# Kernel optimization log

Measured on AMD Instinct MI355X. Metric: run time of the kernel, lower is better.

Reference implementation:

```python
import jax, jax.numpy as jnp
import numpy as np

DIMS = 1024; HEAD = 16; HD = DIMS // HEAD
MAX_DIST = 1024; MAX_SPAN = 1024; TEMP_SCALE = 0.01
SCALE = HD ** -0.25  # hd^-0.25 per the torch modules


def _layer_norm(x, g, b, eps=1e-5):
    m = jnp.mean(x, -1, keepdims=True)
    v = jnp.mean((x - m) ** 2, -1, keepdims=True)
    return (x - m) * jax.lax.rsqrt(v + eps) * g + b


def _forward(x, ln_a_g, ln_a_b, ln_b_g, ln_b_b, Wq, bq, Wk, Wv, bv, Wc, bc, Wp, bp, Wo, bo):
    B, S, D = x.shape
    local = _layer_norm(x, ln_a_g, ln_a_b)
    globe = _layer_norm(x, ln_b_g, ln_b_b)
    # --- global path: QueryModule/KeyModule/ValueModule + AttentionCombiner SDPA (mask=None) ---
    q = (globe @ Wq.T + bq).reshape(B, S, HEAD, HD).transpose(0, 2, 1, 3) * SCALE
    k = (globe @ Wk.T).reshape(B, S, HEAD, HD).transpose(0, 2, 1, 3) * SCALE
    v = (globe @ Wv.T + bv).reshape(B, S, HEAD, HD).transpose(0, 2, 1, 3)
    # SDPA applies its own 1/sqrt(hd) on top of the modules' hd^-0.25 scalings (faithful to torch)
    scores = jnp.einsum('bhqd,bhkd->bhqk', q, k) / jnp.sqrt(jnp.asarray(HD, x.dtype))
    w = jax.nn.softmax(scores, -1)
    g_out = jnp.einsum('bhqk,bhkd->bhqd', w, v).transpose(0, 2, 1, 3).reshape(B, S, D)
    g_out = g_out @ Wc.T + bc
    # --- span predictor; torch uses span_scale.mean().item() which detaches -> stop_gradient ---
    span_scale = jax.nn.sigmoid(jnp.mean(g_out, 1) @ Wp.T + bp)  # [B,1]
    span_mean = jax.lax.stop_gradient(jnp.mean(span_scale))
    span_len = jnp.minimum(jnp.floor(MAX_SPAN * span_mean).astype(jnp.int32), S)
    eff = jnp.maximum(jnp.minimum(span_len, MAX_DIST), 1)  # eff_span (>=1 to keep softmax finite)
    temp = 1.0 + TEMP_SCALE * (1.0 - span_mean)  # sharpen=True branch
    # --- local AdaptiveSpan path: q[:, :eff], k[:, :eff], v[:, :eff] expressed as masking
    #     so shapes stay static under jit; rows >= eff are the zero-padding of the span output.
    lh = local.reshape(B, S, HEAD, HD).transpose(0, 2, 1, 3)  # [B,H,S,hd]
    ls = jnp.einsum('bhqd,bhkd->bhqk', lh, lh) / temp * SCALE
    valid = jnp.arange(S) < eff
    ls = jnp.where(valid[None, None, None, :], ls, jnp.asarray(-1e30, x.dtype))
    lw = jax.nn.softmax(ls, -1)
    l_out = jnp.einsum('bhqk,bhkd->bhqd', lw, lh).transpose(0, 2, 1, 3).reshape(B, S, D)
    l_out = jnp.where(valid[None, :, None], l_out, jnp.asarray(0.0, x.dtype))
    combined = jnp.concatenate([l_out, g_out], -1)  # [B,S,2D]
    return combined @ Wo.T + bo


def setup_inputs() -> dict:
    key = jax.random.key(0)
    ks = jax.random.split(key, 8)
    B, S = 2, 1024
    nrm = lambda k, sh, std=0.02: jax.random.normal(k, sh, jnp.float32) * std
    return {
        'x': jax.random.normal(ks[0], (B, S, DIMS), jnp.float32),
        'ln_a_g': jnp.ones(DIMS, jnp.float32), 'ln_a_b': jnp.zeros(DIMS, jnp.float32),
        'ln_b_g': jnp.ones(DIMS, jnp.float32), 'ln_b_b': jnp.zeros(DIMS, jnp.float32),
        'Wq': nrm(ks[1], (DIMS, DIMS)), 'bq': jnp.zeros(DIMS, jnp.float32),
        'Wk': nrm(ks[2], (DIMS, DIMS)),
        'Wv': nrm(ks[3], (DIMS, DIMS)), 'bv': jnp.zeros(DIMS, jnp.float32),
        'Wc': nrm(ks[4], (DIMS, DIMS)), 'bc': jnp.zeros(DIMS, jnp.float32),
        'Wp': nrm(ks[5], (1, DIMS), (2.0 / (DIMS + 1)) ** 0.5), 'bp': jnp.zeros(1, jnp.float32),
        'Wo': nrm(ks[6], (DIMS, 2 * DIMS)), 'bo': jnp.zeros(DIMS, jnp.float32),
    }


def reference(x, ln_a_g, ln_a_b, ln_b_g, ln_b_b, Wq, bq, Wk, Wv, bv, Wc, bc, Wp, bp, Wo, bo):
    return _forward(x, ln_a_g, ln_a_b, ln_b_g, ln_b_b, Wq, bq, Wk, Wv, bv, Wc, bc, Wp, bp, Wo, bo)
```

## Files before the change

kernel.cpp:

```cpp
#include <hip/hip_runtime.h>
#include <math.h>

#define S_LEN 1024
#define DIMS  1024
#define NHEAD 16
#define HD    64
#define BATCH 2
#define MROWS (BATCH * S_LEN)

typedef unsigned short us;
typedef __attribute__((ext_vector_type(8))) __bf16 bf8_t;
typedef __attribute__((ext_vector_type(8))) unsigned short us8_t;
typedef __attribute__((ext_vector_type(4))) unsigned short us4_t;
typedef __attribute__((ext_vector_type(4))) float f32x4;

static __device__ inline us f2bf(float f) {
    unsigned int u = __builtin_bit_cast(unsigned int, f);
    unsigned int r = u + 0x7fffu + ((u >> 16) & 1u);
    return (us)(r >> 16);
}
static __device__ inline float bf2f(us v) {
    unsigned int u = ((unsigned int)v) << 16;
    return __builtin_bit_cast(float, u);
}
static __device__ inline f32x4 mfma16(us8_t a, us8_t b, f32x4 c) {
    return __builtin_amdgcn_mfma_f32_16x16x32_bf16(
        __builtin_bit_cast(bf8_t, a), __builtin_bit_cast(bf8_t, b), c, 0, 0, 0);
}

__global__ __launch_bounds__(256) void cvt5_kernel(
    const float* __restrict__ s0, const float* __restrict__ s1,
    const float* __restrict__ s2, const float* __restrict__ s3,
    const float* __restrict__ s4,
    us* __restrict__ d0, us* __restrict__ d1, us* __restrict__ d2,
    us* __restrict__ d3, us* __restrict__ d4)
{
    int bidx = blockIdx.x;
    const float* src; us* dst; int blk;
    if (bidx < 1024)      { src = s0; dst = d0; blk = bidx; }
    else if (bidx < 2048) { src = s1; dst = d1; blk = bidx - 1024; }
    else if (bidx < 3072) { src = s2; dst = d2; blk = bidx - 2048; }
    else if (bidx < 4096) { src = s3; dst = d3; blk = bidx - 3072; }
    else                  { src = s4; dst = d4; blk = bidx - 4096; }
    size_t idx = (size_t)blk * 1024 + threadIdx.x * 4;
    float4 v = *(const float4*)(src + idx);
    us4_t ot;
    ot[0] = f2bf(v.x); ot[1] = f2bf(v.y); ot[2] = f2bf(v.z); ot[3] = f2bf(v.w);
    *(us4_t*)(dst + idx) = ot;
}

__global__ __launch_bounds__(256) void ln2_kernel(
    const float* __restrict__ x,
    const float* __restrict__ ga, const float* __restrict__ ba,
    const float* __restrict__ gb, const float* __restrict__ bb,
    us* __restrict__ outA, us* __restrict__ outB)
{
    int row = blockIdx.x;
    int t = threadIdx.x;
    const float* xr = x + (size_t)row * DIMS;
    float4 v = *(const float4*)(xr + t * 4);
    float s  = v.x + v.y + v.z + v.w;
    float s2 = v.x * v.x + v.y * v.y + v.z * v.z + v.w * v.w;
#pragma unroll
    for (int o = 32; o > 0; o >>= 1) {
        s  += __shfl_down(s, o, 64);
        s2 += __shfl_down(s2, o, 64);
    }
    __shared__ float rs[4], rs2[4];
    int wid = t >> 6, lane = t & 63;
    if (lane == 0) { rs[wid] = s; rs2[wid] = s2; }
    __syncthreads();
    float S0 = rs[0] + rs[1] + rs[2] + rs[3];
    float S2 = rs2[0] + rs2[1] + rs2[2] + rs2[3];
    float mean = S0 * (1.0f / DIMS);
    float var  = S2 * (1.0f / DIMS) - mean * mean;
    float inv  = 1.0f / sqrtf(var + 1e-5f);
    float4 vga = *(const float4*)(ga + t * 4);
    float4 vba = *(const float4*)(ba + t * 4);
    float4 vgb = *(const float4*)(gb + t * 4);
    float4 vbb = *(const float4*)(bb + t * 4);
    float nx = (v.x - mean) * inv, ny = (v.y - mean) * inv;
    float nz = (v.z - mean) * inv, nw = (v.w - mean) * inv;
    us4_t oa, ob;
    oa[0] = f2bf(nx * vga.x + vba.x); oa[1] = f2bf(ny * vga.y + vba.y);
    oa[2] = f2bf(nz * vga.z + vba.z); oa[3] = f2bf(nw * vga.w + vba.w);
    ob[0] = f2bf(nx * vgb.x + vbb.x); ob[1] = f2bf(ny * vgb.y + vbb.y);
    ob[2] = f2bf(nz * vgb.z + vbb.z); ob[3] = f2bf(nw * vgb.w + vbb.w);
    *(us4_t*)(outA + (size_t)row * DIMS + t * 4) = oa;
    *(us4_t*)(outB + (size_t)row * DIMS + t * 4) = ob;
}

template <int OUTBF>
static __device__ __forceinline__ void gemm_body(
    const us* __restrict__ A, int lda,
    const us* __restrict__ W, int ldw,
    const float* __restrict__ bias,
    void* __restrict__ Cp, int ldc, int K,
    int bm, int bn, us* As, us* Bs)
{
    int tid = threadIdx.x;
    int w = tid >> 6, l = tid & 63, l15 = l & 15, lhi = l >> 4;
    int wr = w >> 1, wc = w & 1;
    f32x4 acc[2][2] = {{{0,0,0,0},{0,0,0,0}},{{0,0,0,0},{0,0,0,0}}};
    int srow = tid >> 3;
    int scol8 = tid & 7;
    const us* Ap = A + (size_t)(bm + srow) * lda + scol8 * 8;
    const us* Wpt = W + (size_t)(bn + srow) * ldw + scol8 * 8;
    int sl = (scol8 ^ (srow & 7)) * 8;
    us8_t a0 = *(const us8_t*)(Ap);
    us8_t a1 = *(const us8_t*)(Ap + (size_t)32 * lda);
    us8_t b0 = *(const us8_t*)(Wpt);
    us8_t b1 = *(const us8_t*)(Wpt + (size_t)32 * ldw);
    for (int kt = 0; kt < K; kt += 64) {
        __syncthreads();
        *(us8_t*)&As[srow * 64 + sl] = a0;
        *(us8_t*)&As[(srow + 32) * 64 + sl] = a1;
        *(us8_t*)&Bs[srow * 64 + sl] = b0;
        *(us8_t*)&Bs[(srow + 32) * 64 + sl] = b1;
        __syncthreads();
        if (kt + 64 < K) {
            a0 = *(const us8_t*)(Ap + kt + 64);
            a1 = *(const us8_t*)(Ap + (size_t)32 * lda + kt + 64);
            b0 = *(const us8_t*)(Wpt + kt + 64);
            b1 = *(const us8_t*)(Wpt + (size_t)32 * ldw + kt + 64);
        }
#pragma unroll
        for (int kk = 0; kk < 2; ++kk) {
            us8_t af[2], bfr[2];
#pragma unroll
            for (int m = 0; m < 2; ++m) {
                int rowm = wr * 32 + m * 16 + l15;
                af[m] = *(const us8_t*)&As[rowm * 64 + (((kk * 4 + lhi)) ^ (rowm & 7)) * 8];
            }
#pragma unroll
            for (int n = 0; n < 2; ++n) {
                int rown = wc * 32 + n * 16 + l15;
                bfr[n] = *(const us8_t*)&Bs[rown * 64 + (((kk * 4 + lhi)) ^ (rown & 7)) * 8];
            }
#pragma unroll
            for (int m = 0; m < 2; ++m)
#pragma unroll
                for (int n = 0; n < 2; ++n)
                    acc[m][n] = mfma16(af[m], bfr[n], acc[m][n]);
        }
    }
    float bvv[2] = {0.f, 0.f};
    if (bias) {
#pragma unroll
        for (int n = 0; n < 2; ++n)
            bvv[n] = bias[bn + wc * 32 + n * 16 + l15];
    }
#pragma unroll
    for (int m = 0; m < 2; ++m) {
#pragma unroll
        for (int n = 0; n < 2; ++n) {
#pragma unroll
            for (int r = 0; r < 4; ++r) {
                int row = bm + wr * 32 + m * 16 + lhi * 4 + r;
                int col = bn + wc * 32 + n * 16 + l15;
                float val = acc[m][n][r] + bvv[n];
                if (OUTBF) ((us*)Cp)[(size_t)row * ldc + col] = f2bf(val);
                else       ((float*)Cp)[(size_t)row * ldc + col] = val;
            }
        }
    }
}

template <int OUTBF>
__global__ __launch_bounds__(256) void gemm_bf16(
    const us* __restrict__ A, int lda,
    const us* __restrict__ W, int ldw,
    const float* __restrict__ bias,
    void* __restrict__ Cp, int ldc, int K)
{
    __shared__ __align__(16) us As[64 * 64];
    __shared__ __align__(16) us Bs[64 * 64];
    gemm_body<OUTBF>(A, lda, W, ldw, bias, Cp, ldc, K,
                     blockIdx.y * 64, blockIdx.x * 64, As, Bs);
}

__global__ __launch_bounds__(256) void gemm_qkv(
    const us* __restrict__ A,
    const us* __restrict__ Wq, const us* __restrict__ Wk, const us* __restrict__ Wv,
    const float* __restrict__ bq, const float* __restrict__ bv,
    us* __restrict__ qo, us* __restrict__ ko, us* __restrict__ vo)
{
    __shared__ __align__(16) us As[64 * 64];
    __shared__ __align__(16) us Bs[64 * 64];
    int which = blockIdx.x >> 4;
    int bn = (blockIdx.x & 15) * 64, bm = blockIdx.y * 64;
    const us* W = (which == 0) ? Wq : ((which == 1) ? Wk : Wv);
    const float* bias = (which == 0) ? bq : ((which == 2) ? bv : nullptr);
    us* Out = (which == 0) ? qo : ((which == 1) ? ko : vo);
    gemm_body<1>(A, DIMS, W, DIMS, bias, Out, DIMS, DIMS, bm, bn, As, Bs);
}

template <int LOCAL>
__global__ __launch_bounds__(512) void attn_mfma(
    const us* __restrict__ Q, const us* __restrict__ K,
    const us* __restrict__ V, us* __restrict__ O, int ldo,
    const float* __restrict__ span)
{
    __shared__ __align__(16) us Ks[2][64 * 64];
    __shared__ __align__(16) us Vt[2][64 * 64];
    __shared__ __align__(16) us Ps[8][16 * 64];

    int b = blockIdx.z, h = blockIdx.y;
    int q0blk = blockIdx.x * 64;
    int tid = threadIdx.x;
    int w = tid >> 6, l = tid & 63;
    int l15 = l & 15, lhi = l >> 4;
    int wq = w & 3, wk = w >> 2;

    float scale; int eff;
    if (LOCAL) { scale = span[1]; eff = (int)span[0]; }
    else       { scale = 1.0f / 64.0f; eff = S_LEN; }
    int ntiles = LOCAL ? ((eff + 63) >> 6) : 16;
    int nIter = (ntiles + 1) >> 1;

    int qrow = q0blk + wq * 16 + l15;
    const us* qptr = Q + ((size_t)(b * S_LEN + qrow)) * DIMS + h * HD + lhi * 8;
    us8_t qf[2];
    qf[0] = *(const us8_t*)(qptr);
    qf[1] = *(const us8_t*)(qptr + 32);

    f32x4 o[4] = {{0,0,0,0},{0,0,0,0},{0,0,0,0},{0,0,0,0}};
    float m_r[4] = {-1e30f, -1e30f, -1e30f, -1e30f};
    float l_r[4] = {0.f, 0.f, 0.f, 0.f};

    int half = tid >> 8;
    int t0 = tid & 255;
    int krow = t0 >> 3, kcol8 = t0 & 7;
    int ksl = (kcol8 ^ (krow & 7)) * 8;
    int vkb = t0 & 15, vdb = t0 >> 4;
    const us* Kb = K + ((size_t)(b * S_LEN)) * DIMS + h * HD;
    const us* Vb = V + ((size_t)(b * S_LEN)) * DIMS + h * HD;

    us8_t kc0, kc1;
    us4_t vr0, vr1, vr2, vr3;
    if (half < ntiles) {
        const us* kp = Kb + (size_t)(half * 64 + krow) * DIMS + kcol8 * 8;
        kc0 = *(const us8_t*)kp;
        kc1 = *(const us8_t*)(kp + (size_t)32 * DIMS);
        const us* vp = Vb + (size_t)(half * 64 + vkb * 4) * DIMS + vdb * 4;
        vr0 = *(const us4_t*)(vp);
        vr1 = *(const us4_t*)(vp + DIMS);
        vr2 = *(const us4_t*)(vp + 2 * DIMS);
        vr3 = *(const us4_t*)(vp + 3 * DIMS);
    }

    for (int i = 0; i < nIter; ++i) {
        __syncthreads();
        if (2 * i + half < ntiles) {
            *(us8_t*)&Ks[half][krow * 64 + ksl] = kc0;
            *(us8_t*)&Ks[half][(krow + 32) * 64 + ksl] = kc1;
#pragma unroll
            for (int j = 0; j < 4; ++j) {
                int d = vdb * 4 + j;
                us4_t wv;
                wv[0] = vr0[j]; wv[1] = vr1[j]; wv[2] = vr2[j]; wv[3] = vr3[j];
                int slot = (vkb >> 1) ^ (d & 7);
                *(us4_t*)&Vt[half][d * 64 + slot * 8 + (vkb & 1) * 4] = wv;
            }
        }
        __syncthreads();
        int nt2 = 2 * (i + 1) + half;
        if (nt2 < ntiles) {
            const us* kp = Kb + (size_t)(nt2 * 64 + krow) * DIMS + kcol8 * 8;
            kc0 = *(const us8_t*)kp;
            kc1 = *(const us8_t*)(kp + (size_t)32 * DIMS);
            const us* vp = Vb + (size_t)(nt2 * 64 + vkb * 4) * DIMS + vdb * 4;
            vr0 = *(const us4_t*)(vp);
            vr1 = *(const us4_t*)(vp + DIMS);
            vr2 = *(const us4_t*)(vp + 2 * DIMS);
            vr3 = *(const us4_t*)(vp + 3 * DIMS);
        }
        int kt = 2 * i + wk;
        if (kt < ntiles) {
            f32x4 s4[4] = {{0,0,0,0},{0,0,0,0},{0,0,0,0},{0,0,0,0}};
            __builtin_amdgcn_s_setprio(1);
#pragma unroll
            for (int kk = 0; kk < 2; ++kk) {
#pragma unroll
                for (int n = 0; n < 4; ++n) {
                    int key = n * 16 + l15;
                    int slot = (kk * 4 + lhi) ^ (key & 7);
                    us8_t bk = *(const us8_t*)&Ks[wk][key * 64 + slot * 8];
                    s4[n] = mfma16(qf[kk], bk, s4[n]);
                }
            }
            __builtin_amdgcn_s_setprio(0);
#pragma unroll
            for (int n = 0; n < 4; ++n) {
                s4[n] *= scale;
                if (LOCAL) {
                    int key = kt * 64 + n * 16 + l15;
                    if (key >= eff) {
                        s4[n][0] = -1e30f; s4[n][1] = -1e30f;
                        s4[n][2] = -1e30f; s4[n][3] = -1e30f;
                    }
                }
            }
            float tm[4];
#pragma unroll
            for (int r = 0; r < 4; ++r)
                tm[r] = fmaxf(fmaxf(s4[0][r], s4[1][r]), fmaxf(s4[2][r], s4[3][r]));
#pragma unroll
            for (int msk = 1; msk <= 8; msk <<= 1) {
#pragma unroll
                for (int r = 0; r < 4; ++r)
                    tm[r] = fmaxf(tm[r], __shfl_xor(tm[r], msk, 64));
            }
            bool upd = (tm[0] > m_r[0] + 8.f) || (tm[1] > m_r[1] + 8.f) ||
                       (tm[2] > m_r[2] + 8.f) || (tm[3] > m_r[3] + 8.f);
            if (upd) {
                float fac[4];
#pragma unroll
                for (int r = 0; r < 4; ++r) {
                    float mn = fmaxf(m_r[r], tm[r]);
                    fac[r] = __expf(m_r[r] - mn);
                    m_r[r] = mn;
                    l_r[r] *= fac[r];
                }
#pragma unroll
                for (int n = 0; n < 4; ++n) {
                    o[n][0] *= fac[0]; o[n][1] *= fac[1];
                    o[n][2] *= fac[2]; o[n][3] *= fac[3];
                }
            }
            float ladd[4] = {0.f, 0.f, 0.f, 0.f};
#pragma unroll
            for (int n = 0; n < 4; ++n) {
                int col = n * 16 + l15;
                int slotbase = col >> 3;
#pragma unroll
                for (int r = 0; r < 4; ++r) {
                    float p = __expf(s4[n][r] - m_r[r]);
                    ladd[r] += p;
                    int qlr = lhi * 4 + r;
                    int slot = slotbase ^ (qlr & 7);
                    Ps[w][qlr * 64 + slot * 8 + (col & 7)] = f2bf(p);
                }
            }
#pragma unroll
            for (int msk = 1; msk <= 8; msk <<= 1) {
#pragma unroll
                for (int r = 0; r < 4; ++r)
                    ladd[r] += __shfl_xor(ladd[r], msk, 64);
            }
#pragma unroll
            for (int r = 0; r < 4; ++r) l_r[r] += ladd[r];

            __builtin_amdgcn_s_setprio(1);
#pragma unroll
            for (int kk = 0; kk < 2; ++kk) {
                int slot = (kk * 4 + lhi) ^ (l15 & 7);
                us8_t pa = *(const us8_t*)&Ps[w][l15 * 64 + slot * 8];
#pragma unroll
                for (int n = 0; n < 4; ++n) {
                    int d = n * 16 + l15;
                    int vslot = (kk * 4 + lhi) ^ (d & 7);
                    us8_t vb = *(const us8_t*)&Vt[wk][d * 64 + vslot * 8];
                    o[n] = mfma16(pa, vb, o[n]);
                }
            }
            __builtin_amdgcn_s_setprio(0);
        }
    }

    __syncthreads();
    float* obuf = (float*)&Ks[0][0];
    float* mlb  = (float*)&Vt[0][0];
    if (wk == 1) {
#pragma unroll
        for (int n = 0; n < 4; ++n)
#pragma unroll
            for (int r = 0; r < 4; ++r)
                obuf[wq * 1024 + (lhi * 4 + r) * 64 + n * 16 + l15] = o[n][r];
        if (l15 == 0) {
#pragma unroll
            for (int r = 0; r < 4; ++r) {
                mlb[wq * 32 + (lhi * 4 + r) * 2 + 0] = m_r[r];
                mlb[wq * 32 + (lhi * 4 + r) * 2 + 1] = l_r[r];
            }
        }
    }
    __syncthreads();
    if (wk == 0) {
        float f0[4], f1[4], rcp[4];
#pragma unroll
        for (int r = 0; r < 4; ++r) {
            int row = lhi * 4 + r;
            float m1 = mlb[wq * 32 + row * 2 + 0];
            float l1 = mlb[wq * 32 + row * 2 + 1];
            float ms = fmaxf(m_r[r], m1);
            f0[r] = __expf(m_r[r] - ms);
            f1[r] = __expf(m1 - ms);
            rcp[r] = 1.0f / (l_r[r] * f0[r] + l1 * f1[r]);
        }
#pragma unroll
        for (int n = 0; n < 4; ++n) {
#pragma unroll
            for (int r = 0; r < 4; ++r) {
                int row = q0blk + wq * 16 + lhi * 4 + r;
                float val = (o[n][r] * f0[r] +
                             obuf[wq * 1024 + (lhi * 4 + r) * 64 + n * 16 + l15] * f1[r]) * rcp[r];
                if (LOCAL && row >= eff) val = 0.0f;
                O[((size_t)(b * S_LEN + row)) * ldo + h * HD + n * 16 + l15] = f2bf(val);
            }
        }
    }
}

__global__ __launch_bounds__(256) void span1_kernel(
    const us* __restrict__ gout, const float* __restrict__ Wp,
    float* __restrict__ partials)
{
    int slice = blockIdx.x;
    int b = blockIdx.y;
    int t = threadIdx.x;
    float4 wp = *(const float4*)(Wp + t * 4);
    float acc = 0;
    int s0 = slice * 128;
    for (int s = s0; s < s0 + 128; ++s) {
        us4_t g = *(const us4_t*)(gout + (size_t)(b * S_LEN + s) * 2048 + t * 4);
        acc += bf2f(g[0]) * wp.x + bf2f(g[1]) * wp.y + bf2f(g[2]) * wp.z + bf2f(g[3]) * wp.w;
    }
#pragma unroll
    for (int o = 32; o > 0; o >>= 1) acc += __shfl_down(acc, o, 64);
    __shared__ float r[4];
    int wid = t >> 6, lane = t & 63;
    if (lane == 0) r[wid] = acc;
    __syncthreads();
    if (t == 0) partials[b * 8 + slice] = r[0] + r[1] + r[2] + r[3];
}

__global__ void span2_kernel(const float* __restrict__ partials,
                             const float* __restrict__ bp,
                             float* __restrict__ spanbuf)
{
    if (threadIdx.x == 0 && blockIdx.x == 0) {
        float l0 = 0, l1 = 0;
        for (int i = 0; i < 8; ++i) { l0 += partials[i]; l1 += partials[8 + i]; }
        l0 = l0 * (1.0f / 1024.0f) + bp[0];
        l1 = l1 * (1.0f / 1024.0f) + bp[0];
        float s0 = 1.0f / (1.0f + expf(-l0));
        float s1 = 1.0f / (1.0f + expf(-l1));
        float sm = 0.5f * (s0 + s1);
        int sl = (int)floorf(1024.0f * sm);
        int eff = sl; if (eff > 1024) eff = 1024; if (eff < 1) eff = 1;
        float temp = 1.0f + 0.01f * (1.0f - sm);
        spanbuf[0] = (float)eff;
        spanbuf[1] = 0.35355339059327378f / temp;
    }
}

extern "C" void kernel_launch(void* const* d_in, const int* in_sizes, int n_in,
                              void* d_out, int out_size, void* d_ws, size_t ws_size,
                              hipStream_t stream)
{
    (void)in_sizes; (void)n_in; (void)out_size; (void)ws_size;
    const float* x   = (const float*)d_in[0];
    const float* lag = (const float*)d_in[1];
    const float* lab = (const float*)d_in[2];
    const float* lbg = (const float*)d_in[3];
    const float* lbb = (const float*)d_in[4];
    const float* Wq  = (const float*)d_in[5];
    const float* bq  = (const float*)d_in[6];
    const float* Wk  = (const float*)d_in[7];
    const float* Wv  = (const float*)d_in[8];
    const float* bv  = (const float*)d_in[9];
    const float* Wc  = (const float*)d_in[10];
    const float* bc  = (const float*)d_in[11];
    const float* Wp  = (const float*)d_in[12];
    const float* bp  = (const float*)d_in[13];
    const float* Wo  = (const float*)d_in[14];
    const float* bo  = (const float*)d_in[15];
    float* out = (float*)d_out;
    us* wsu = (us*)d_ws;

    const size_t NM = (size_t)MROWS * DIMS;
    us* lnAbf = wsu;
    us* lnBbf = wsu + NM;
    us* gattbf = lnBbf;
    us* qbf   = wsu + 2 * NM;
    us* kbf   = wsu + 3 * NM;
    us* vbf   = wsu + 4 * NM;
    us* combbf = qbf;
    us* Wqbf  = wsu + 5 * NM;
    us* Wkbf  = Wqbf + DIMS * DIMS;
    us* Wvbf  = Wkbf + DIMS * DIMS;
    us* Wcbf  = Wvbf + DIMS * DIMS;
    us* Wobf  = Wcbf + DIMS * DIMS;
    float* partials = (float*)(Wobf + 2 * DIMS * DIMS);
    float* spanbuf  = partials + 16;

    cvt5_kernel<<<6144, 256, 0, stream>>>(Wq, Wk, Wv, Wc, Wo,
                                          Wqbf, Wkbf, Wvbf, Wcbf, Wobf);

    ln2_kernel<<<MROWS, 256, 0, stream>>>(x, lag, lab, lbg, lbb, lnAbf, lnBbf);

    gemm_qkv<<<dim3(48, MROWS / 64), 256, 0, stream>>>(
        lnBbf, Wqbf, Wkbf, Wvbf, bq, bv, qbf, kbf, vbf);

    dim3 ag(S_LEN / 64, NHEAD, BATCH);
    attn_mfma<0><<<ag, 512, 0, stream>>>(qbf, kbf, vbf, gattbf, DIMS, nullptr);

    dim3 gg(DIMS / 64, MROWS / 64);
    gemm_bf16<1><<<gg, 256, 0, stream>>>(gattbf, DIMS, Wcbf, DIMS, bc, combbf + 1024, 2048, DIMS);

    span1_kernel<<<dim3(8, BATCH), 256, 0, stream>>>(combbf + 1024, Wp, partials);
    span2_kernel<<<1, 64, 0, stream>>>(partials, bp, spanbuf);

    attn_mfma<1><<<ag, 512, 0, stream>>>(lnAbf, lnAbf, lnAbf, combbf, 2048, spanbuf);

    gemm_bf16<0><<<gg, 256, 0, stream>>>(combbf, 2048, Wobf, 2048, bo, out, DIMS, 2 * DIMS);
}
```

Before: 142.2 us.

## Use 128-row GEMM tiles, exp2 softmax, packed bf16 converts, deferred row-sum reduction

Adds a 128x64 GEMM tile variant and uses it for the QKV and output projections, so each block reuses its weight tile across twice as many rows. In attention, the scale is folded with log2(e) so softmax can use exp2, and the lazy-rescale threshold is adjusted to match. The per-tile cross-lane row-sum shuffle is moved to a single reduction after the loop. Fp32-to-bf16 conversion now uses the packed v_cvt_pk_bf16_f32 instruction, and swizzle address arithmetic is simplified. The larger tiles halve the block count and raise register pressure, which may lower occupancy.

Result: no change. 143.7 us (+1.1%).

```diff
diff --git a/kernel.cpp b/kernel.cpp
--- a/kernel.cpp
+++ b/kernel.cpp
@@ -7,6 +7,7 @@
 #define HD    64
 #define BATCH 2
 #define MROWS (BATCH * S_LEN)
+#define LOG2E 1.44269504088896f
 
 typedef unsigned short us;
 typedef __attribute__((ext_vector_type(8))) __bf16 bf8_t;
@@ -22,6 +23,11 @@
 static __device__ inline float bf2f(us v) {
     unsigned int u = ((unsigned int)v) << 16;
     return __builtin_bit_cast(float, u);
+}
+static __device__ inline unsigned int pk2bf(float lo, float hi) {
+    unsigned int r;
+    asm("v_cvt_pk_bf16_f32 %0, %1, %2" : "=v"(r) : "v"(lo), "v"(hi));
+    return r;
 }
 static __device__ inline f32x4 mfma16(us8_t a, us8_t b, f32x4 c) {
     return __builtin_amdgcn_mfma_f32_16x16x32_bf16(
@@ -91,7 +97,7 @@
 }
 
 template <int OUTBF>
-static __device__ __forceinline__ void gemm_body(
+static __device__ __forceinline__ void gemm128_body(
     const us* __restrict__ A, int lda,
     const us* __restrict__ W, int ldw,
     const float* __restrict__ bias,
@@ -101,6 +107,127 @@
     int tid = threadIdx.x;
     int w = tid >> 6, l = tid & 63, l15 = l & 15, lhi = l >> 4;
     int wr = w >> 1, wc = w & 1;
+    f32x4 acc[4][2];
+#pragma unroll
+    for (int m = 0; m < 4; ++m) { acc[m][0] = (f32x4){0,0,0,0}; acc[m][1] = (f32x4){0,0,0,0}; }
+    int srow = tid >> 3;
+    int scol8 = tid & 7;
+    int sl = (scol8 ^ (srow & 7)) * 8;
+    const us* Ap = A + (size_t)(bm + srow) * lda + scol8 * 8;
+    const us* Wpt = W + (size_t)(bn + srow) * ldw + scol8 * 8;
+    us8_t a0 = *(const us8_t*)(Ap);
+    us8_t a1 = *(const us8_t*)(Ap + (size_t)32 * lda);
+    us8_t a2 = *(const us8_t*)(Ap + (size_t)64 * lda);
+    us8_t a3 = *(const us8_t*)(Ap + (size_t)96 * lda);
+    us8_t b0 = *(const us8_t*)(Wpt);
+    us8_t b1 = *(const us8_t*)(Wpt + (size_t)32 * ldw);
+    int xorbase = l15 & 7;
+    for (int kt = 0; kt < K; kt += 64) {
+        __syncthreads();
+        *(us8_t*)&As[(srow +  0) * 64 + sl] = a0;
+        *(us8_t*)&As[(srow + 32) * 64 + sl] = a1;
+        *(us8_t*)&As[(srow + 64) * 64 + sl] = a2;
+        *(us8_t*)&As[(srow + 96) * 64 + sl] = a3;
+        *(us8_t*)&Bs[(srow +  0) * 64 + sl] = b0;
+        *(us8_t*)&Bs[(srow + 32) * 64 + sl] = b1;
+        __syncthreads();
+        if (kt + 64 < K) {
+            a0 = *(const us8_t*)(Ap + kt + 64);
+            a1 = *(const us8_t*)(Ap + (size_t)32 * lda + kt + 64);
+            a2 = *(const us8_t*)(Ap + (size_t)64 * lda + kt + 64);
+            a3 = *(const us8_t*)(Ap + (size_t)96 * lda + kt + 64);
+            b0 = *(const us8_t*)(Wpt + kt + 64);
+            b1 = *(const us8_t*)(Wpt + (size_t)32 * ldw + kt + 64);
+        }
+#pragma unroll
+        for (int kk = 0; kk < 2; ++kk) {
+            int xo = ((kk * 4 + lhi) ^ xorbase) * 8;
+            us8_t af[4], bfr[2];
+#pragma unroll
+            for (int m = 0; m < 4; ++m)
+                af[m] = *(const us8_t*)&As[(wr * 64 + m * 16 + l15) * 64 + xo];
+#pragma unroll
+            for (int n = 0; n < 2; ++n)
+                bfr[n] = *(const us8_t*)&Bs[(wc * 32 + n * 16 + l15) * 64 + xo];
+#pragma unroll
+            for (int m = 0; m < 4; ++m)
+#pragma unroll
+                for (int n = 0; n < 2; ++n)
+                    acc[m][n] = mfma16(af[m], bfr[n], acc[m][n]);
+        }
+    }
+    float bvv[2] = {0.f, 0.f};
+    if (bias) {
+#pragma unroll
+        for (int n = 0; n < 2; ++n)
+            bvv[n] = bias[bn + wc * 32 + n * 16 + l15];
+    }
+#pragma unroll
+    for (int m = 0; m < 4; ++m) {
+#pragma unroll
+        for (int n = 0; n < 2; ++n) {
+            int row = bm + wr * 64 + m * 16 + lhi * 4;
+            int col = bn + wc * 32 + n * 16 + l15;
+            if (OUTBF) {
+                us* Cb = (us*)Cp;
+                unsigned int p01 = pk2bf(acc[m][n][0] + bvv[n], acc[m][n][1] + bvv[n]);
+                unsigned int p23 = pk2bf(acc[m][n][2] + bvv[n], acc[m][n][3] + bvv[n]);
+                Cb[(size_t)(row + 0) * ldc + col] = (us)p01;
+                Cb[(size_t)(row + 1) * ldc + col] = (us)(p01 >> 16);
+                Cb[(size_t)(row + 2) * ldc + col] = (us)p23;
+                Cb[(size_t)(row + 3) * ldc + col] = (us)(p23 >> 16);
+            } else {
+                float* Cf = (float*)Cp;
+#pragma unroll
+                for (int r = 0; r < 4; ++r)
+                    Cf[(size_t)(row + r) * ldc + col] = acc[m][n][r] + bvv[n];
+            }
+        }
+    }
+}
+
+template <int OUTBF>
+__global__ __launch_bounds__(256) void gemm128(
+    const us* __restrict__ A, int lda,
+    const us* __restrict__ W, int ldw,
+    const float* __restrict__ bias,
+    void* __restrict__ Cp, int ldc, int K)
+{
+    __shared__ __align__(16) us As[128 * 64];
+    __shared__ __align__(16) us Bs[64 * 64];
+    gemm128_body<OUTBF>(A, lda, W, ldw, bias, Cp, ldc, K,
+                        blockIdx.y * 128, blockIdx.x * 64, As, Bs);
+}
+
+__global__ __launch_bounds__(256) void gemm_qkv(
+    const us* __restrict__ A,
+    const us* __restrict__ Wq, const us* __restrict__ Wk, const us* __restrict__ Wv,
+    const float* __restrict__ bq, const float* __restrict__ bv,
+    us* __restrict__ qo, us* __restrict__ ko, us* __restrict__ vo)
+{
+    __shared__ __align__(16) us As[128 * 64];
+    __shared__ __align__(16) us Bs[64 * 64];
+    int which = blockIdx.x >> 4;
+    int bn = (blockIdx.x & 15) * 64, bm = blockIdx.y * 128;
+    const us* W = (which == 0) ? Wq : ((which == 1) ? Wk : Wv);
+    const float* bias = (which == 0) ? bq : ((which == 2) ? bv : nullptr);
+    us* Out = (which == 0) ? qo : ((which == 1) ? ko : vo);
+    gemm128_body<1>(A, DIMS, W, DIMS, bias, Out, DIMS, DIMS, bm, bn, As, Bs);
+}
+
+template <int OUTBF>
+__global__ __launch_bounds__(256) void gemm_bf16(
+    const us* __restrict__ A, int lda,
+    const us* __restrict__ W, int ldw,
+    const float* __restrict__ bias,
+    void* __restrict__ Cp, int ldc, int K)
+{
+    __shared__ __align__(16) us As[64 * 64];
+    __shared__ __align__(16) us Bs[64 * 64];
+    int tid = threadIdx.x;
+    int w = tid >> 6, l = tid & 63, l15 = l & 15, lhi = l >> 4;
+    int wr = w >> 1, wc = w & 1;
+    int bm = blockIdx.y * 64, bn = blockIdx.x * 64;
     f32x4 acc[2][2] = {{{0,0,0,0},{0,0,0,0}},{{0,0,0,0},{0,0,0,0}}};
     int srow = tid >> 3;
     int scol8 = tid & 7;
@@ -111,6 +238,7 @@
     us8_t a1 = *(const us8_t*)(Ap + (size_t)32 * lda);
     us8_t b0 = *(const us8_t*)(Wpt);
     us8_t b1 = *(const us8_t*)(Wpt + (size_t)32 * ldw);
+    int xorbase = l15 & 7;
     for (int kt = 0; kt < K; kt += 64) {
         __syncthreads();
         *(us8_t*)&As[srow * 64 + sl] = a0;
@@ -126,17 +254,14 @@
         }
 #pragma unroll
         for (int kk = 0; kk < 2; ++kk) {
+            int xo = ((kk * 4 + lhi) ^ xorbase) * 8;
             us8_t af[2], bfr[2];
 #pragma unroll
-            for (int m = 0; m < 2; ++m) {
-                int rowm = wr * 32 + m * 16 + l15;
-                af[m] = *(const us8_t*)&As[rowm * 64 + (((kk * 4 + lhi)) ^ (rowm & 7)) * 8];
-            }
-#pragma unroll
-            for (int n = 0; n < 2; ++n) {
-                int rown = wc * 32 + n * 16 + l15;
-                bfr[n] = *(const us8_t*)&Bs[rown * 64 + (((kk * 4 + lhi)) ^ (rown & 7)) * 8];
-            }
+            for (int m = 0; m < 2; ++m)
+                af[m] = *(const us8_t*)&As[(wr * 32 + m * 16 + l15) * 64 + xo];
+#pragma unroll
+            for (int n = 0; n < 2; ++n)
+                bfr[n] = *(const us8_t*)&Bs[(wc * 32 + n * 16 + l15) * 64 + xo];
 #pragma unroll
             for (int m = 0; m < 2; ++m)
 #pragma unroll
@@ -154,45 +279,24 @@
     for (int m = 0; m < 2; ++m) {
 #pragma unroll
         for (int n = 0; n < 2; ++n) {
-#pragma unroll
-            for (int r = 0; r < 4; ++r) {
-                int row = bm + wr * 32 + m * 16 + lhi * 4 + r;
-                int col = bn + wc * 32 + n * 16 + l15;
-                float val = acc[m][n][r] + bvv[n];
-                if (OUTBF) ((us*)Cp)[(size_t)row * ldc + col] = f2bf(val);
-                else       ((float*)Cp)[(size_t)row * ldc + col] = val;
-            }
-        }
-    }
-}
-
-template <int OUTBF>
-__global__ __launch_bounds__(256) void gemm_bf16(
-    const us* __restrict__ A, int lda,
-    const us* __restrict__ W, int ldw,
-    const float* __restrict__ bias,
-    void* __restrict__ Cp, int ldc, int K)
-{
-    __shared__ __align__(16) us As[64 * 64];
-    __shared__ __align__(16) us Bs[64 * 64];
-    gemm_body<OUTBF>(A, lda, W, ldw, bias, Cp, ldc, K,
-                     blockIdx.y * 64, blockIdx.x * 64, As, Bs);
-}
-
-__global__ __launch_bounds__(256) void gemm_qkv(
-    const us* __restrict__ A,
-    const us* __restrict__ Wq, const us* __restrict__ Wk, const us* __restrict__ Wv,
-    const float* __restrict__ bq, const float* __restrict__ bv,
-    us* __restrict__ qo, us* __restrict__ ko, us* __restrict__ vo)
-{
-    __shared__ __align__(16) us As[64 * 64];
-    __shared__ __align__(16) us Bs[64 * 64];
-    int which = blockIdx.x >> 4;
-    int bn = (blockIdx.x & 15) * 64, bm = blockIdx.y * 64;
-    const us* W = (which == 0) ? Wq : ((which == 1) ? Wk : Wv);
-    const float* bias = (which == 0) ? bq : ((which == 2) ? bv : nullptr);
-    us* Out = (which == 0) ? qo : ((which == 1) ? ko : vo);
-    gemm_body<1>(A, DIMS, W, DIMS, bias, Out, DIMS, DIMS, bm, bn, As, Bs);
+            int row = bm + wr * 32 + m * 16 + lhi * 4;
+            int col = bn + wc * 32 + n * 16 + l15;
+            if (OUTBF) {
+                us* Cb = (us*)Cp;
+                unsigned int p01 = pk2bf(acc[m][n][0] + bvv[n], acc[m][n][1] + bvv[n]);
+                unsigned int p23 = pk2bf(acc[m][n][2] + bvv[n], acc[m][n][3] + bvv[n]);
+                Cb[(size_t)(row + 0) * ldc + col] = (us)p01;
+                Cb[(size_t)(row + 1) * ldc + col] = (us)(p01 >> 16);
+                Cb[(size_t)(row + 2) * ldc + col] = (us)p23;
+                Cb[(size_t)(row + 3) * ldc + col] = (us)(p23 >> 16);
+            } else {
+                float* Cf = (float*)Cp;
+#pragma unroll
+                for (int r = 0; r < 4; ++r)
+                    Cf[(size_t)(row + r) * ldc + col] = acc[m][n][r] + bvv[n];
+            }
+        }
+    }
 }
 
 template <int LOCAL>
@@ -213,8 +317,8 @@
     int wq = w & 3, wk = w >> 2;
 
     float scale; int eff;
-    if (LOCAL) { scale = span[1]; eff = (int)span[0]; }
-    else       { scale = 1.0f / 64.0f; eff = S_LEN; }
+    if (LOCAL) { scale = span[1] * LOG2E; eff = (int)span[0]; }
+    else       { scale = LOG2E / 64.0f; eff = S_LEN; }
     int ntiles = LOCAL ? ((eff + 63) >> 6) : 16;
     int nIter = (ntiles + 1) >> 1;
 
@@ -281,11 +385,10 @@
             __builtin_amdgcn_s_setprio(1);
 #pragma unroll
             for (int kk = 0; kk < 2; ++kk) {
+                int xo = ((kk * 4 + lhi) ^ (l15 & 7)) * 8;
 #pragma unroll
                 for (int n = 0; n < 4; ++n) {
-                    int key = n * 16 + l15;
-                    int slot = (kk * 4 + lhi) ^ (key & 7);
-                    us8_t bk = *(const us8_t*)&Ks[wk][key * 64 + slot * 8];
+                    us8_t bk = *(const us8_t*)&Ks[wk][(n * 16 + l15) * 64 + xo];
                     s4[n] = mfma16(qf[kk], bk, s4[n]);
                 }
             }
@@ -311,14 +414,14 @@
                 for (int r = 0; r < 4; ++r)
                     tm[r] = fmaxf(tm[r], __shfl_xor(tm[r], msk, 64));
             }
-            bool upd = (tm[0] > m_r[0] + 8.f) || (tm[1] > m_r[1] + 8.f) ||
-                       (tm[2] > m_r[2] + 8.f) || (tm[3] > m_r[3] + 8.f);
+            bool upd = (tm[0] > m_r[0] + 11.5f) || (tm[1] > m_r[1] + 11.5f) ||
+                       (tm[2] > m_r[2] + 11.5f) || (tm[3] > m_r[3] + 11.5f);
             if (upd) {
                 float fac[4];
 #pragma unroll
                 for (int r = 0; r < 4; ++r) {
                     float mn = fmaxf(m_r[r], tm[r]);
-                    fac[r] = __expf(m_r[r] - mn);
+                    fac[r] = exp2f(m_r[r] - mn);
                     m_r[r] = mn;
                     l_r[r] *= fac[r];
                 }
@@ -328,44 +431,43 @@
                     o[n][2] *= fac[2]; o[n][3] *= fac[3];
                 }
             }
-            float ladd[4] = {0.f, 0.f, 0.f, 0.f};
 #pragma unroll
             for (int n = 0; n < 4; ++n) {
                 int col = n * 16 + l15;
                 int slotbase = col >> 3;
-#pragma unroll
-                for (int r = 0; r < 4; ++r) {
-                    float p = __expf(s4[n][r] - m_r[r]);
-                    ladd[r] += p;
-                    int qlr = lhi * 4 + r;
-                    int slot = slotbase ^ (qlr & 7);
-                    Ps[w][qlr * 64 + slot * 8 + (col & 7)] = f2bf(p);
-                }
-            }
-#pragma unroll
-            for (int msk = 1; msk <= 8; msk <<= 1) {
-#pragma unroll
-                for (int r = 0; r < 4; ++r)
-                    ladd[r] += __shfl_xor(ladd[r], msk, 64);
-            }
-#pragma unroll
-            for (int r = 0; r < 4; ++r) l_r[r] += ladd[r];
-
+                float p0 = exp2f(s4[n][0] - m_r[0]);
+                float p1 = exp2f(s4[n][1] - m_r[1]);
+                float p2 = exp2f(s4[n][2] - m_r[2]);
+                float p3 = exp2f(s4[n][3] - m_r[3]);
+                l_r[0] += p0; l_r[1] += p1; l_r[2] += p2; l_r[3] += p3;
+                unsigned int p01 = pk2bf(p0, p1);
+                unsigned int p23 = pk2bf(p2, p3);
+                int q0 = lhi * 4;
+                Ps[w][(q0 + 0) * 64 + ((slotbase ^ ((q0 + 0) & 7)) * 8) + (col & 7)] = (us)p01;
+                Ps[w][(q0 + 1) * 64 + ((slotbase ^ ((q0 + 1) & 7)) * 8) + (col & 7)] = (us)(p01 >> 16);
+                Ps[w][(q0 + 2) * 64 + ((slotbase ^ ((q0 + 2) & 7)) * 8) + (col & 7)] = (us)p23;
+                Ps[w][(q0 + 3) * 64 + ((slotbase ^ ((q0 + 3) & 7)) * 8) + (col & 7)] = (us)(p23 >> 16);
+            }
             __builtin_amdgcn_s_setprio(1);
 #pragma unroll
             for (int kk = 0; kk < 2; ++kk) {
-                int slot = (kk * 4 + lhi) ^ (l15 & 7);
-                us8_t pa = *(const us8_t*)&Ps[w][l15 * 64 + slot * 8];
+                int xo = ((kk * 4 + lhi) ^ (l15 & 7)) * 8;
+                us8_t pa = *(const us8_t*)&Ps[w][l15 * 64 + ((kk * 4 + lhi) ^ (l15 & 7)) * 8];
 #pragma unroll
                 for (int n = 0; n < 4; ++n) {
-                    int d = n * 16 + l15;
-                    int vslot = (kk * 4 + lhi) ^ (d & 7);
-                    us8_t vb = *(const us8_t*)&Vt[wk][d * 64 + vslot * 8];
+                    us8_t vb = *(const us8_t*)&Vt[wk][(n * 16 + l15) * 64 + xo];
                     o[n] = mfma16(pa, vb, o[n]);
                 }
             }
             __builtin_amdgcn_s_setprio(0);
         }
+    }
+
+#pragma unroll
+    for (int msk = 1; msk <= 8; msk <<= 1) {
+#pragma unroll
+        for (int r = 0; r < 4; ++r)
+            l_r[r] += __shfl_xor(l_r[r], msk, 64);
     }
 
     __syncthreads();
@@ -394,20 +496,29 @@
             float m1 = mlb[wq * 32 + row * 2 + 0];
             float l1 = mlb[wq * 32 + row * 2 + 1];
             float ms = fmaxf(m_r[r], m1);
-            f0[r] = __expf(m_r[r] - ms);
-            f1[r] = __expf(m1 - ms);
+            f0[r] = exp2f(m_r[r] - ms);
+            f1[r] = exp2f(m1 - ms);
             rcp[r] = 1.0f / (l_r[r] * f0[r] + l1 * f1[r]);
         }
 #pragma unroll
         for (int n = 0; n < 4; ++n) {
+            float vv[4];
 #pragma unroll
             for (int r = 0; r < 4; ++r) {
                 int row = q0blk + wq * 16 + lhi * 4 + r;
                 float val = (o[n][r] * f0[r] +
                              obuf[wq * 1024 + (lhi * 4 + r) * 64 + n * 16 + l15] * f1[r]) * rcp[r];
                 if (LOCAL && row >= eff) val = 0.0f;
-                O[((size_t)(b * S_LEN + row)) * ldo + h * HD + n * 16 + l15] = f2bf(val);
-            }
+                vv[r] = val;
+            }
+            int row0 = q0blk + wq * 16 + lhi * 4;
+            unsigned int p01 = pk2bf(vv[0], vv[1]);
+            unsigned int p23 = pk2bf(vv[2], vv[3]);
+            size_t base = ((size_t)(b * S_LEN + row0)) * ldo + h * HD + n * 16 + l15;
+            O[base + 0 * ldo] = (us)p01;
+            O[base + 1 * ldo] = (us)(p01 >> 16);
+            O[base + 2 * ldo] = (us)p23;
+            O[base + 3 * ldo] = (us)(p23 >> 16);
         }
     }
 }
@@ -500,19 +611,20 @@
 
     ln2_kernel<<<MROWS, 256, 0, stream>>>(x, lag, lab, lbg, lbb, lnAbf, lnBbf);
 
-    gemm_qkv<<<dim3(48, MROWS / 64), 256, 0, stream>>>(
+    gemm_qkv<<<dim3(48, MROWS / 128), 256, 0, stream>>>(
         lnBbf, Wqbf, Wkbf, Wvbf, bq, bv, qbf, kbf, vbf);
 
     dim3 ag(S_LEN / 64, NHEAD, BATCH);
     attn_mfma<0><<<ag, 512, 0, stream>>>(qbf, kbf, vbf, gattbf, DIMS, nullptr);
 
-    dim3 gg(DIMS / 64, MROWS / 64);
-    gemm_bf16<1><<<gg, 256, 0, stream>>>(gattbf, DIMS, Wcbf, DIMS, bc, combbf + 1024, 2048, DIMS);
+    gemm_bf16<1><<<dim3(DIMS / 64, MROWS / 64), 256, 0, stream>>>(
+        gattbf, DIMS, Wcbf, DIMS, bc, combbf + 1024, 2048, DIMS);
 
     span1_kernel<<<dim3(8, BATCH), 256, 0, stream>>>(combbf + 1024, Wp, partials);
     span2_kernel<<<1, 64, 0, stream>>>(partials, bp, spanbuf);
 
     attn_mfma<1><<<ag, 512, 0, stream>>>(lnAbf, lnAbf, lnAbf, combbf, 2048, spanbuf);
 
-    gemm_bf16<0><<<gg, 256, 0, stream>>>(combbf, 2048, Wobf, 2048, bo, out, DIMS, 2 * DIMS);
-}
+    gemm128<0><<<dim3(DIMS / 64, MROWS / 128), 256, 0, stream>>>(
+        combbf, 2048, Wobf, 2048, bo, out, DIMS, 2 * DIMS);
+}
```
